# Kernel optimization log

Measured on AMD Instinct MI355X. Metric: run time of the kernel, lower is better.

## Reference

```python
import jax, jax.numpy as jnp
import numpy as np

D = 200; K = 10; NHEAD = 5; HDIM = 40; ANS = 2; THRESH = 0.4; GHEAD = 5; GC = 2
B = 8; L = 80; R = 64

def _lin(x, W, b):
    return x @ W + b

def _ln(x, g, b):
    m = jnp.mean(x, -1, keepdims=True)
    v = jnp.var(x, -1, keepdims=True)
    return (x - m) / jnp.sqrt(v + 1e-5) * g + b

def _sparsemax(z):
    # sparsemax along last axis (Martins & Astudillo)
    zs = -jnp.sort(-z, axis=-1)
    k = jnp.arange(1, z.shape[-1] + 1, dtype=z.dtype)
    cs = jnp.cumsum(zs, -1)
    supp = jnp.sum((1.0 + k * zs) > cs, -1, keepdims=True)
    tau = (jnp.take_along_axis(cs, supp - 1, -1) - 1.0) / supp.astype(z.dtype)
    return jnp.maximum(z - tau, 0.0)

def _pair(a, b):
    # a [B,n,d], b [B,m,d] -> [B,n*m,4d] feature cat [a, b, a*b, a-b]
    Bn, n, d = a.shape; m = b.shape[1]
    a1 = jnp.broadcast_to(a[:, :, None, :], (Bn, n, m, d))
    b1 = jnp.broadcast_to(b[:, None, :, :], (Bn, n, m, d))
    return jnp.concatenate([a1, b1, a1 * b1, a1 - b1], -1).reshape(Bn, n * m, 4 * d)

def _topk_sel(E, s, mask):
    # select top-K instances by score (masked)
    s = jnp.where(mask, s, -jnp.inf)
    _, idx = jax.lax.top_k(s, K)
    return jnp.take_along_axis(E, idx[:, :, None], axis=1)

def _mco(x, W_attn, b_attn, W_ff1, b_ff1, W_ff2, b_ff2, ln_g, ln_b):
    # transformer encoder layer: MHA + FFN, post-norm (dropout off at eval)
    Bn, N, d = x.shape
    q = _lin(x, W_attn[0], b_attn[0]).reshape(Bn, N, NHEAD, HDIM)
    k = _lin(x, W_attn[1], b_attn[1]).reshape(Bn, N, NHEAD, HDIM)
    v = _lin(x, W_attn[2], b_attn[2]).reshape(Bn, N, NHEAD, HDIM)
    att = jax.nn.softmax(jnp.einsum('bnhk,bmhk->bhnm', q, k) / np.float32(np.sqrt(HDIM)), axis=-1)
    o = jnp.einsum('bhnm,bmhk->bnhk', att, v).reshape(Bn, N, d)
    x = _ln(x + _lin(o, W_attn[3], b_attn[3]), ln_g[0], ln_b[0])
    f = _lin(jax.nn.relu(_lin(x, W_ff1, b_ff1)), W_ff2, b_ff2)
    return _ln(x + f, ln_g[1], ln_b[1])

def _forward(imgs, encoded_texts, mask_T, mask_TT, mask_TV, adj,
             answer_set, Wt, bt, Wi1, bi1, Wi2, bi2, Wgc, bgc, Wps, bps, Wts, bts,
             W_single, b_single, W_pair1, b_pair1, W_pair2, b_pair2, W_topk, b_topk,
             clues, W_clue1, b_clue1, W_ans1, b_ans1, W_inst2, b_inst2, W_ans2, b_ans2,
             W_attn, b_attn, W_ff1, b_ff1, W_ff2, b_ff2, ln_g, ln_b,
             W_guide, b_guide, W_at1, b_at1, W_at2, b_at2):
    imgs_0 = jax.nn.relu(_lin(jax.nn.relu(_lin(imgs, Wi1, bi1)), Wi2, bi2))  # ImageEncoder 768->500->200
    texts_0 = _lin(encoded_texts, Wt, bt)                                    # TextEncoder 768->200
    Bn, l, _ = texts_0.shape
    r = imgs_0.shape[1]
    ones_V = jnp.ones((Bn, r), bool)
    ones_VV = jnp.ones((Bn, r * r), bool)
    out = []
    for gc_i in range(GC):
        def pair_mlp(f, i):
            return jax.nn.relu(_lin(jax.nn.relu(_lin(f, W_pair1[i], b_pair1[i])), W_pair2[i], b_pair2[i]))
        def score(E, i):
            return jax.nn.relu(E @ W_topk[i] + b_topk[i])
        # five modality streams
        E_T = jax.nn.relu(_lin(texts_0, W_single[0], b_single[0]))
        E_V = jax.nn.relu(_lin(imgs_0, W_single[1], b_single[1]))
        E_TT = pair_mlp(_pair(texts_0, texts_0), 0)
        E_TV = pair_mlp(_pair(texts_0, imgs_0), 1)
        E_VV = pair_mlp(_pair(imgs_0, imgs_0), 2)
        E_T_k = _topk_sel(E_T, score(E_T, 0), mask_T)
        E_V_k = _topk_sel(E_V, score(E_V, 1), ones_V)
        E_TT_k = _topk_sel(E_TT, score(E_TT, 2), mask_TT)
        E_TV_k = _topk_sel(E_TV, score(E_TV, 3), mask_TV)
        E_VV_k = _topk_sel(E_VV, score(E_VV, 4), ones_VV)
        # clue binding: attend selected instances onto per-stream clue banks, condition on answer set
        ans1 = _lin(answer_set, W_ans1, b_ans1)
        def bind(Ek, c):
            att = jax.nn.softmax(jnp.einsum('bkd,cd->bkc', Ek, c), -1)
            bound = jnp.einsum('bkc,cd->bkd', att, c)
            return jax.nn.relu(_lin(bound, W_clue1, b_clue1)[:, :, None, :] + ans1[None, None])
        preds = jnp.concatenate([bind(E_T_k, clues[0]), bind(E_V_k, clues[1]), bind(E_TT_k, clues[2]), bind(E_TV_k, clues[3]), bind(E_VV_k, clues[4])], axis=1)  # [B,5K,A,D]
        E_cat = jnp.concatenate([E_T_k, E_V_k, E_TT_k, E_TV_k, E_VV_k], 1)
        E4 = jnp.broadcast_to(E_cat[:, :, None, :], preds.shape)
        inst_score = jnp.einsum('bnad,ad->bna', _lin(E4, W_inst2, b_inst2), _lin(answer_set, W_ans2, b_ans2))
        preds_ = jnp.stack([_mco(preds[:, :, a, :], W_attn, b_attn, W_ff1, b_ff1, W_ff2, b_ff2, ln_g, ln_b) for a in range(ANS)], axis=2)
        feat = jnp.concatenate([E4, preds, E4 - preds, E4 * preds], -1)
        atoms = jax.nn.sigmoid(_lin(jax.nn.relu(_lin(feat, W_at1, b_at1)), W_at2, b_at2))[..., 0]
        atoms = jnp.transpose(atoms, (2, 0, 1))  # [A,B,5K]
        # global text/image embeddings for guide scores
        I_score = jax.nn.softmax(imgs_0 @ Wps + bps, -1)
        T_score = jax.nn.softmax(texts_0 @ Wts + bts, -1)
        I_emb = jnp.einsum('brd,br->bd', imgs_0, I_score)
        T_emb = jnp.einsum('bld,bl->bd', texts_0, T_score)
        E_IT = pair_mlp(jnp.concatenate([T_emb, I_emb, T_emb * I_emb, T_emb - I_emb], -1), 1)
        heads = []
        for gi in range(GHEAD):
            g1 = jnp.einsum('bnad,d->bna', preds_, W_guide[2 * gi]) + b_guide[2 * gi]
            g2 = (E_IT @ W_guide[2 * gi + 1] + b_guide[2 * gi + 1])[:, None, None]
            fcs = _sparsemax(g1 * g2) * _sparsemax(inst_score)
            fcs = _sparsemax(jnp.transpose(fcs, (2, 0, 1)))  # [A,B,5K], sparsemax over instances
            flag = fcs >= THRESH
            mprod = jnp.prod(jnp.where(flag, atoms, 1.0), -1)  # conjunction over selected atoms
            vals, idx = jax.lax.top_k(fcs, 3)                  # fallback: top-3 atoms weighted by score
            fb = jnp.prod(jnp.take_along_axis(atoms, idx, -1) * vals, -1)
            heads.append(jnp.where(jnp.any(flag, -1), mprod, fb))  # [A,B]
        out.append(jnp.max(jnp.stack(heads, -1), -1))  # max over guide heads -> [A,B]
        # graph convolution refines text+image node features for next iteration
        graph = jnp.concatenate([texts_0, imgs_0], 1)
        graph = jax.nn.relu(jnp.einsum('bnm,bmd->bnd', adj, graph) @ Wgc[gc_i] + bgc[gc_i])
        texts_0 = graph[:, :l, :]
        imgs_0 = graph[:, l:, :]
    return jnp.stack(out)  # [GC, A, B]

def setup_inputs():
    ks = jax.random.split(jax.random.key(0), 64)
    def rn(i, shape, s=0.05):
        return jax.random.normal(ks[i], shape, dtype=jnp.float32) * s
    inp = {}
    inp['imgs'] = rn(0, (B, R, 768), 1.0)
    inp['encoded_texts'] = rn(1, (B, L, 768), 1.0)
    inp['mask_batch_T'] = jnp.ones((B, L), dtype=bool)
    inp['mask_batch_TT'] = jnp.ones((B, L * L), dtype=bool)
    inp['mask_batch_TV'] = jnp.ones((B, L * R), dtype=bool)
    inp['adj_matrix'] = jax.random.uniform(ks[2], (B, L + R, L + R), dtype=jnp.float32) / (L + R)
    inp['word_len'] = jax.random.randint(ks[3], (B,), 1, L)
    inp['word_spans'] = jax.random.randint(ks[4], (B, L, 2), 0, L)
    inp['answer_set'] = rn(5, (ANS, D), 0.5)
    inp['Wt'] = rn(6, (768, D)); inp['bt'] = rn(7, (D,))
    inp['Wi1'] = rn(8, (768, 500)); inp['bi1'] = rn(9, (500,))
    inp['Wi2'] = rn(10, (500, D)); inp['bi2'] = rn(11, (D,))
    inp['Wgc'] = rn(12, (GC, D, D)); inp['bgc'] = rn(13, (GC, D))
    inp['Wps'] = rn(14, (D,), 0.5); inp['bps'] = rn(15, ())
    inp['Wts'] = rn(16, (D,), 0.5); inp['bts'] = rn(17, ())
    inp['W_single'] = rn(18, (2, D, D)); inp['b_single'] = rn(19, (2, D))
    inp['W_pair1'] = rn(20, (3, 4 * D, 2 * D)); inp['b_pair1'] = rn(21, (3, 2 * D))
    inp['W_pair2'] = rn(22, (3, 2 * D, D)); inp['b_pair2'] = rn(23, (3, D))
    inp['W_topk'] = rn(24, (5, D), 0.5); inp['b_topk'] = rn(25, (5,))
    inp['clues'] = rn(26, (5, 5, D), 0.5)
    inp['W_clue1'] = rn(27, (D, D)); inp['b_clue1'] = rn(28, (D,))
    inp['W_ans1'] = rn(29, (D, D)); inp['b_ans1'] = rn(30, (D,))
    inp['W_inst2'] = rn(31, (D, D)); inp['b_inst2'] = rn(32, (D,))
    inp['W_ans2'] = rn(33, (D, D)); inp['b_ans2'] = rn(34, (D,))
    inp['W_attn'] = rn(35, (4, D, D)); inp['b_attn'] = rn(36, (4, D))
    inp['W_ff1'] = rn(37, (D, 2 * D)); inp['b_ff1'] = rn(38, (2 * D,))
    inp['W_ff2'] = rn(39, (2 * D, D)); inp['b_ff2'] = rn(40, (D,))
    inp['ln_g'] = jnp.ones((2, D), jnp.float32); inp['ln_b'] = jnp.zeros((2, D), jnp.float32)
    inp['W_guide'] = rn(41, (2 * GHEAD, D), 0.5); inp['b_guide'] = rn(42, (2 * GHEAD,))
    inp['W_at1'] = rn(43, (4 * D, 2 * D)); inp['b_at1'] = rn(44, (2 * D,))
    inp['W_at2'] = rn(45, (2 * D, 1)); inp['b_at2'] = rn(46, (1,))
    return inp

def reference(imgs, encoded_texts, mask_batch_T, mask_batch_TT, mask_batch_TV, adj_matrix, word_len, word_spans,
              answer_set, Wt, bt, Wi1, bi1, Wi2, bi2, Wgc, bgc, Wps, bps, Wts, bts,
              W_single, b_single, W_pair1, b_pair1, W_pair2, b_pair2, W_topk, b_topk,
              clues, W_clue1, b_clue1, W_ans1, b_ans1, W_inst2, b_inst2, W_ans2, b_ans2,
              W_attn, b_attn, W_ff1, b_ff1, W_ff2, b_ff2, ln_g, ln_b,
              W_guide, b_guide, W_at1, b_at1, W_at2, b_at2):
    # word_len / word_spans are consumed by the (simplified) TextEncoder pooling; not needed here
    return _forward(imgs, encoded_texts, mask_batch_T, mask_batch_TT, mask_batch_TV, adj_matrix,
                    answer_set, Wt, bt, Wi1, bi1, Wi2, bi2, Wgc, bgc, Wps, bps, Wts, bts,
                    W_single, b_single, W_pair1, b_pair1, W_pair2, b_pair2, W_topk, b_topk,
                    clues, W_clue1, b_clue1, W_ans1, b_ans1, W_inst2, b_inst2, W_ans2, b_ans2,
                    W_attn, b_attn, W_ff1, b_ff1, W_ff2, b_ff2, ln_g, ln_b,
                    W_guide, b_guide, W_at1, b_at1, W_at2, b_at2)
```

## Files before the change

kernel.cpp:

```cpp
#include <hip/hip_runtime.h>
#include <hip/hip_bf16.h>


__device__ __forceinline__ void sparsemax2(float z0, float z1, float& o0, float& o1) {
  float S0 = (z1 > z0) ? z1 : 0.f;
  float S1 = (z0 > z1) ? z0 : 0.f;
  float cz0 = (z1 > z0) ? z0 : 0.f;
  float cz1 = (z0 > z1) ? z1 : 0.f;
  bool c0 = (1.f + cz0) > S0;
  bool c1 = (1.f + cz1) > S1;
  float supp = (c0 ? 1.f : 0.f) + (c1 ? 1.f : 0.f);
  float Ss   = (c0 ? z0  : 0.f) + (c1 ? z1  : 0.f);
  float tau = (Ss - 1.f) / supp;
  o0 = fmaxf(z0 - tau, 0.f);
  o1 = fmaxf(z1 - tau, 0.f);
}

__global__ __launch_bounds__(256) void gemm_k(
    const float* __restrict__ A, const float* __restrict__ Bw,
    const float* __restrict__ bias, float* __restrict__ C,
    int M, int N, int K, long sA, long sB, long sC, int act)
{
  int batch = blockIdx.z;
  A  += (long)batch * sA;
  Bw += (long)batch * sB;
  C  += (long)batch * sC;
  __shared__ float As[32][33];
  __shared__ float Bs[32][33];
  int tid = threadIdx.x;
  int tx = tid & 15, ty = tid >> 4;
  int row0 = blockIdx.y * 32, col0 = blockIdx.x * 32;
  float acc00 = 0.f, acc01 = 0.f, acc10 = 0.f, acc11 = 0.f;
  for (int k0 = 0; k0 < K; k0 += 32) {
    for (int i = tid; i < 1024; i += 256) {
      int r = i >> 5, c = i & 31;
      int ar = row0 + r, ac = k0 + c;
      As[r][c] = (ar < M && ac < K) ? A[(long)ar * K + ac] : 0.f;
      int br = k0 + r, bc = col0 + c;
      Bs[r][c] = (br < K && bc < N) ? Bw[(long)br * N + bc] : 0.f;
    }
    __syncthreads();
#pragma unroll
    for (int kk = 0; kk < 32; ++kk) {
      float a0 = As[ty * 2][kk], a1 = As[ty * 2 + 1][kk];
      float b0 = Bs[kk][tx * 2], b1 = Bs[kk][tx * 2 + 1];
      acc00 += a0 * b0; acc01 += a0 * b1; acc10 += a1 * b0; acc11 += a1 * b1;
    }
    __syncthreads();
  }
  int r0 = row0 + ty * 2, c0 = col0 + tx * 2;
#define STORE_(rr, cc, v)                                        \
  if ((rr) < M && (cc) < N) {                                    \
    float t_ = (v) + (bias ? bias[cc] : 0.f);                    \
    if (act) t_ = fmaxf(t_, 0.f);                                \
    C[(long)(rr) * N + (cc)] = t_;                               \
  }
  STORE_(r0, c0, acc00); STORE_(r0, c0 + 1, acc01);
  STORE_(r0 + 1, c0, acc10); STORE_(r0 + 1, c0 + 1, acc11);
#undef STORE_
}

__global__ void wab_kernel(const float* __restrict__ P1, float* __restrict__ Wa,
                           float* __restrict__ Wb) {
  int idx = blockIdx.x * 256 + threadIdx.x;
  if (idx >= 240000) return;
  int t = idx / 80000, r2 = idx % 80000;
  int d = r2 / 400, k = r2 % 400;
  long base = (long)t * 320000;
  float wd = P1[base + (long)(600 + d) * 400 + k];
  Wa[idx] = P1[base + (long)d * 400 + k] + wd;
  Wb[idx] = P1[base + (long)(200 + d) * 400 + k] - wd;
}

__global__ void ans_kernel(const float* __restrict__ as, const float* __restrict__ W1,
                           const float* __restrict__ b1, const float* __restrict__ W2,
                           const float* __restrict__ b2, float* __restrict__ ans1,
                           float* __restrict__ ans2) {
  int idx = blockIdx.x * 256 + threadIdx.x;
  if (idx >= 400) return;
  int a = idx / 200, d = idx % 200;
  float a1 = b1[d], a2 = b2[d];
  for (int k = 0; k < 200; ++k) {
    float av = as[a * 200 + k];
    a1 += av * W1[k * 200 + d];
    a2 += av * W2[k * 200 + d];
  }
  ans1[idx] = a1;
  ans2[idx] = a2;
}

__global__ void rowdot_kernel(const float* __restrict__ E, const float* __restrict__ Wt,
                              const float* __restrict__ bt, int g, float* __restrict__ s,
                              int rows) {
  int r = blockIdx.x * 256 + threadIdx.x;
  if (r >= rows) return;
  const float* e = E + (long)r * 200;
  const float* w = Wt + g * 200;
  float acc = bt[g];
  for (int d = 0; d < 200; ++d) acc += e[d] * w[d];
  s[r] = fmaxf(acc, 0.f);
}

__global__ __launch_bounds__(256) void pair_score_kernel(
    const float* __restrict__ Arows, int an, const float* __restrict__ Brows, int bm,
    const float* __restrict__ At, const float* __restrict__ Bt,
    const float* __restrict__ Wc, const float* __restrict__ W2,
    const float* __restrict__ b2, const float* __restrict__ wt,
    const float* __restrict__ btk, int gidx, float* __restrict__ scores)
{
  const int tid = threadIdx.x;
  const int b = blockIdx.y;
  const int nTJ = bm >> 3;
  const int i0 = (blockIdx.x / nTJ) * 8;
  const int j0 = (blockIdx.x % nTJ) * 8;

  Arows += (long)b * an * 200;
  Brows += (long)b * bm * 200;
  At += (long)b * an * 400;
  Bt += (long)b * bm * 400;
  scores += (long)b * an * bm;

  __shared__ __align__(16) float pdbuf[13056];
  __shared__ __align__(16) float stg[3200];

  const int tp = tid >> 4;
  const int tk = tid & 15;
  const int tc = tid & 15;

  for (int idx = tid; idx < 12800; idx += 256) {
    int p = idx / 200, d = idx - p * 200;
    pdbuf[p * 204 + d] = Arows[(long)(i0 + (p >> 3)) * 200 + d] *
                         Brows[(long)(j0 + (p & 7)) * 200 + d];
  }

  float acc[4][25];
#pragma unroll
  for (int q = 0; q < 4; ++q)
#pragma unroll
    for (int kk = 0; kk < 25; ++kk) acc[q][kk] = 0.f;

  float wreg[7];
#pragma unroll
  for (int l = 0; l < 7; ++l) {
    int idx = tid + l * 256;
    if (idx < 1600) wreg[l] = Wc[(long)(idx / 400) * 400 + idx % 400];
  }
#pragma unroll
  for (int l = 0; l < 7; ++l) {
    int idx = tid + l * 256;
    if (idx < 1600) stg[idx] = wreg[l];
  }
  __syncthreads();

  for (int ph = 0; ph < 50; ++ph) {
    const int cur = ph & 1, nxt = cur ^ 1;
    if (ph < 49) {
#pragma unroll
      for (int l = 0; l < 7; ++l) {
        int idx = tid + l * 256;
        if (idx < 1600)
          wreg[l] = Wc[(long)((ph + 1) * 4 + idx / 400) * 400 + idx % 400];
      }
    }
    float pdq[4][4];
#pragma unroll
    for (int q = 0; q < 4; ++q) {
      const float4 v = *reinterpret_cast<const float4*>(
          &pdbuf[(tp * 4 + q) * 204 + ph * 4]);
      pdq[q][0] = v.x; pdq[q][1] = v.y; pdq[q][2] = v.z; pdq[q][3] = v.w;
    }
#pragma unroll
    for (int dd = 0; dd < 4; ++dd) {
      const float* wrow = &stg[cur * 1600 + dd * 400 + tk * 25];
#pragma unroll
      for (int kk = 0; kk < 25; ++kk) {
        const float wv = wrow[kk];
        acc[0][kk] = fmaf(pdq[0][dd], wv, acc[0][kk]);
        acc[1][kk] = fmaf(pdq[1][dd], wv, acc[1][kk]);
        acc[2][kk] = fmaf(pdq[2][dd], wv, acc[2][kk]);
        acc[3][kk] = fmaf(pdq[3][dd], wv, acc[3][kk]);
      }
    }
    if (ph < 49) {
#pragma unroll
      for (int l = 0; l < 7; ++l) {
        int idx = tid + l * 256;
        if (idx < 1600) stg[nxt * 1600 + idx] = wreg[l];
      }
    }
    __syncthreads();
  }

  {
    const float* Ar = &At[(long)(i0 + (tp >> 1)) * 400 + tk * 25];
#pragma unroll
    for (int q = 0; q < 4; ++q) {
      const float* Br = &Bt[(long)(j0 + ((tp & 1) * 4 + q)) * 400 + tk * 25];
#pragma unroll
      for (int kk = 0; kk < 25; ++kk)
        acc[q][kk] = fmaxf(acc[q][kk] + Ar[kk] + Br[kk], 0.f);
    }
  }

  float acc2[4][13];
#pragma unroll
  for (int q = 0; q < 4; ++q)
#pragma unroll
    for (int cc = 0; cc < 13; ++cc) acc2[q][cc] = 0.f;

  float4* const H4 = reinterpret_cast<float4*>(pdbuf);

  for (int P = 0; P < 2; ++P) {
    if ((tk >> 3) == P) {
      const int klbase = (tk & 7) * 25;
#pragma unroll
      for (int kk = 0; kk < 25; ++kk) {
        const int kl = klbase + kk;
        float4 hv = make_float4(acc[0][kk], acc[1][kk], acc[2][kk], acc[3][kk]);
        H4[kl * 16 + (tp ^ ((kl & 7) * 2))] = hv;
      }
    }
#pragma unroll
    for (int l = 0; l < 7; ++l) {
      int idx = tid + l * 256;
      if (idx < 1600) {
        int g = idx >= 800, j = idx - g * 800;
        wreg[l] = W2[(long)(P * 200 + g * 4 + (j & 3)) * 200 + (j >> 2)];
      }
    }
#pragma unroll
    for (int l = 0; l < 7; ++l) {
      int idx = tid + l * 256;
      if (idx < 1600) stg[idx] = wreg[l];
    }
    __syncthreads();

    for (int ch = 0; ch < 25; ++ch) {
      const int cur = ch & 1, nxt = cur ^ 1;
      if (ch < 24) {
#pragma unroll
        for (int l = 0; l < 7; ++l) {
          int idx = tid + l * 256;
          if (idx < 1600) {
            int g = idx >= 800, j = idx - g * 800;
            wreg[l] = W2[(long)(P * 200 + (ch + 1) * 8 + g * 4 + (j & 3)) * 200 +
                         (j >> 2)];
          }
        }
      }
#pragma unroll
      for (int g = 0; g < 2; ++g) {
        const int r0 = ch * 8 + g * 4;
        float4 h0 = H4[(r0 + 0) * 16 + (tp ^ (((g * 4 + 0) & 7) * 2))];
        float4 h1 = H4[(r0 + 1) * 16 + (tp ^ (((g * 4 + 1) & 7) * 2))];
        float4 h2 = H4[(r0 + 2) * 16 + (tp ^ (((g * 4 + 2) & 7) * 2))];
        float4 h3 = H4[(r0 + 3) * 16 + (tp ^ (((g * 4 + 3) & 7) * 2))];
        const float4* S4 = reinterpret_cast<const float4*>(&stg[cur * 1600 + g * 800]);
#pragma unroll
        for (int cc = 0; cc < 13; ++cc) {
          if (!(cc == 12 && tc >= 8)) {
            const float4 wv = S4[tc + 16 * cc];
            acc2[0][cc] += h0.x * wv.x + h1.x * wv.y + h2.x * wv.z + h3.x * wv.w;
            acc2[1][cc] += h0.y * wv.x + h1.y * wv.y + h2.y * wv.z + h3.y * wv.w;
            acc2[2][cc] += h0.z * wv.x + h1.z * wv.y + h2.z * wv.z + h3.z * wv.w;
            acc2[3][cc] += h0.w * wv.x + h1.w * wv.y + h2.w * wv.z + h3.w * wv.w;
          }
        }
      }
      if (ch < 24) {
#pragma unroll
        for (int l = 0; l < 7; ++l) {
          int idx = tid + l * 256;
          if (idx < 1600) stg[nxt * 1600 + idx] = wreg[l];
        }
      }
      __syncthreads();
    }
  }

  float part[4] = {0.f, 0.f, 0.f, 0.f};
#pragma unroll
  for (int cc = 0; cc < 13; ++cc) {
    if (!(cc == 12 && tc >= 8)) {
      const int c = tc + 16 * cc;
      const float bb = b2[c], ww = wt[c];
#pragma unroll
      for (int q = 0; q < 4; ++q)
        part[q] += fmaxf(acc2[q][cc] + bb, 0.f) * ww;
    }
  }
#pragma unroll
  for (int off = 1; off < 16; off <<= 1) {
#pragma unroll
    for (int q = 0; q < 4; ++q) part[q] += __shfl_xor(part[q], off, 64);
  }
  if ((tid & 15) == 0) {
    const float bt_ = btk[gidx];
#pragma unroll
    for (int q = 0; q < 4; ++q) {
      const int p = tp * 4 + q;
      scores[(long)(i0 + (p >> 3)) * bm + (j0 + (p & 7))] = fmaxf(part[q] + bt_, 0.f);
    }
  }
}

__global__ void topk_kernel(const float* __restrict__ sT, const float* __restrict__ sV,
                            const float* __restrict__ sTT, const float* __restrict__ sTV,
                            const float* __restrict__ sVV, int* __restrict__ topIdx) {
  int g = blockIdx.x, b = blockIdx.y, tid = threadIdx.x;
  const float* src; int len;
  switch (g) {
    case 0: src = sT + b * 80; len = 80; break;
    case 1: src = sV + b * 64; len = 64; break;
    case 2: src = sTT + b * 6400; len = 6400; break;
    case 3: src = sTV + b * 5120; len = 5120; break;
    default: src = sVV + b * 4096; len = 4096; break;
  }
  __shared__ float sbuf[6400];
  __shared__ float rv[256];
  __shared__ int ri[256];
  for (int i = tid; i < len; i += 256) sbuf[i] = src[i];
  __syncthreads();
  for (int r = 0; r < 10; ++r) {
    float bv = -1e30f; int bi = 0x7fffffff;
    for (int i = tid; i < len; i += 256) {
      float v = sbuf[i];
      if (v > bv) { bv = v; bi = i; }
    }
    rv[tid] = bv; ri[tid] = bi;
    __syncthreads();
    for (int s = 128; s > 0; s >>= 1) {
      if (tid < s) {
        if (rv[tid + s] > rv[tid] || (rv[tid + s] == rv[tid] && ri[tid + s] < ri[tid])) {
          rv[tid] = rv[tid + s]; ri[tid] = ri[tid + s];
        }
      }
      __syncthreads();
    }
    if (tid == 0) {
      topIdx[(g * 8 + b) * 10 + r] = ri[0];
      sbuf[ri[0]] = -1e30f;
    }
    __syncthreads();
  }
}

__global__ void gather_kernel(
    const int* __restrict__ topIdx, const float* __restrict__ ETf,
    const float* __restrict__ EVf, const float* __restrict__ texts0,
    const float* __restrict__ imgs0, const float* __restrict__ AtTT,
    const float* __restrict__ BtTT, const float* __restrict__ AtTV,
    const float* __restrict__ BtTV, const float* __restrict__ AtVV,
    const float* __restrict__ BtVV, const float* __restrict__ W_pair1,
    const float* __restrict__ W_pair2, const float* __restrict__ b_pair2,
    float* __restrict__ E_cat)
{
  int n = blockIdx.x, b = blockIdx.y, tid = threadIdx.x;
  int g = n / 10, r = n % 10;
  int idx = topIdx[(g * 8 + b) * 10 + r];
  float* out = E_cat + ((long)(b * 50 + n)) * 200;
  if (g == 0) {
    for (int d = tid; d < 200; d += 256) out[d] = ETf[((long)(b * 80 + idx)) * 200 + d];
    return;
  }
  if (g == 1) {
    for (int d = tid; d < 200; d += 256) out[d] = EVf[((long)(b * 64 + idx)) * 200 + d];
    return;
  }
  int t = g - 2;
  int m = (t == 0) ? 80 : 64;
  int i = idx / m, j = idx % m;
  const float* ar = (t == 2) ? imgs0 + ((long)(b * 64 + i)) * 200
                             : texts0 + ((long)(b * 80 + i)) * 200;
  const float* br = (t == 0) ? texts0 + ((long)(b * 80 + j)) * 200
                             : imgs0 + ((long)(b * 64 + j)) * 200;
  const float* Atp = ((t == 0) ? AtTT : (t == 1) ? AtTV : AtVV) +
                     ((long)(b * ((t == 2) ? 64 : 80) + i)) * 400;
  const float* Btp = ((t == 0) ? BtTT : (t == 1) ? BtTV : BtVV) +
                     ((long)(b * ((t == 0) ? 80 : 64) + j)) * 400;
  const float* Wc = W_pair1 + (long)t * 320000 + 160000;
  const float* W2 = W_pair2 + (long)t * 80000;
  const float* bb2 = b_pair2 + t * 200;
  __shared__ float pd[200];
  __shared__ float hh[400];
  for (int d = tid; d < 200; d += 256) pd[d] = ar[d] * br[d];
  __syncthreads();
  for (int k = tid; k < 400; k += 256) {
    float acc = Atp[k] + Btp[k];
    for (int d = 0; d < 200; ++d) acc += pd[d] * Wc[(long)d * 400 + k];
    hh[k] = fmaxf(acc, 0.f);
  }
  __syncthreads();
  for (int c = tid; c < 200; c += 256) {
    float acc = bb2[c];
    for (int k = 0; k < 400; ++k) acc += hh[k] * W2[(long)k * 200 + c];
    out[c] = fmaxf(acc, 0.f);
  }
}

__global__ void bind_kernel(const float* __restrict__ E_cat, const float* __restrict__ clues,
                            const float* __restrict__ W_clue1, const float* __restrict__ b_clue1,
                            const float* __restrict__ ans1, const float* __restrict__ W_inst2,
                            const float* __restrict__ b_inst2, const float* __restrict__ ans2,
                            float* __restrict__ preds, float* __restrict__ inst) {
  int n = blockIdx.x, b = blockIdx.y, tid = threadIdx.x;
  int g = n / 10;
  const float* e = E_cat + ((long)(b * 50 + n)) * 200;
  __shared__ float es[200], att[5], bound[200], vv[200], red[256];
  for (int d = tid; d < 200; d += 256) es[d] = e[d];
  __syncthreads();
  if (tid < 5) {
    const float* cl = clues + ((long)(g * 5 + tid)) * 200;
    float acc = 0.f;
    for (int d = 0; d < 200; ++d) acc += es[d] * cl[d];
    att[tid] = acc;
  }
  __syncthreads();
  if (tid == 0) {
    float mx = att[0];
    for (int c = 1; c < 5; ++c) mx = fmaxf(mx, att[c]);
    float s = 0.f;
    for (int c = 0; c < 5; ++c) { att[c] = expf(att[c] - mx); s += att[c]; }
    float inv = 1.f / s;
    for (int c = 0; c < 5; ++c) att[c] *= inv;
  }
  __syncthreads();
  if (tid < 200) {
    float acc = 0.f;
    for (int c = 0; c < 5; ++c) acc += att[c] * clues[((long)(g * 5 + c)) * 200 + tid];
    bound[tid] = acc;
  }
  __syncthreads();
  if (tid < 200) {
    float acc = b_clue1[tid];
    for (int k = 0; k < 200; ++k) acc += bound[k] * W_clue1[(long)k * 200 + tid];
    long rbase = ((long)(b * 50 + n)) * 2;
    preds[(rbase + 0) * 200 + tid] = fmaxf(acc + ans1[tid], 0.f);
    preds[(rbase + 1) * 200 + tid] = fmaxf(acc + ans1[200 + tid], 0.f);
    float a2 = b_inst2[tid];
    for (int k = 0; k < 200; ++k) a2 += es[k] * W_inst2[(long)k * 200 + tid];
    vv[tid] = a2;
  }
  __syncthreads();
  float p0 = 0.f, p1 = 0.f;
  for (int d = tid; d < 200; d += 256) {
    p0 += vv[d] * ans2[d];
    p1 += vv[d] * ans2[200 + d];
  }
  red[tid] = p0; __syncthreads();
  for (int s = 128; s > 0; s >>= 1) { if (tid < s) red[tid] += red[tid + s]; __syncthreads(); }
  if (tid == 0) inst[((long)(b * 50 + n)) * 2 + 0] = red[0];
  __syncthreads();
  red[tid] = p1; __syncthreads();
  for (int s = 128; s > 0; s >>= 1) { if (tid < s) red[tid] += red[tid + s]; __syncthreads(); }
  if (tid == 0) inst[((long)(b * 50 + n)) * 2 + 1] = red[0];
}

__global__ void attn_kernel(const float* __restrict__ Q, const float* __restrict__ K,
                            const float* __restrict__ V, float* __restrict__ O) {
  int h = blockIdx.x, a = blockIdx.y, b = blockIdx.z, tid = threadIdx.x;
  __shared__ float qs[50][40], ks[50][40], vs[50][40], ss[50][52];
  for (int idx = tid; idx < 2000; idx += 256) {
    int n = idx / 40, t = idx % 40;
    long base = ((long)((b * 50 + n) * 2 + a)) * 200 + h * 40 + t;
    qs[n][t] = Q[base]; ks[n][t] = K[base]; vs[n][t] = V[base];
  }
  __syncthreads();
  float sq = sqrtf(40.0f);
  for (int idx = tid; idx < 2500; idx += 256) {
    int n = idx / 50, m = idx % 50;
    float acc = 0.f;
    for (int t = 0; t < 40; ++t) acc += qs[n][t] * ks[m][t];
    ss[n][m] = acc / sq;
  }
  __syncthreads();
  if (tid < 50) {
    float mx = -1e30f;
    for (int m = 0; m < 50; ++m) mx = fmaxf(mx, ss[tid][m]);
    float s = 0.f;
    for (int m = 0; m < 50; ++m) { float e = expf(ss[tid][m] - mx); ss[tid][m] = e; s += e; }
    float inv = 1.f / s;
    for (int m = 0; m < 50; ++m) ss[tid][m] *= inv;
  }
  __syncthreads();
  for (int idx = tid; idx < 2000; idx += 256) {
    int n = idx / 40, t = idx % 40;
    float acc = 0.f;
    for (int m = 0; m < 50; ++m) acc += ss[n][m] * vs[m][t];
    O[((long)((b * 50 + n) * 2 + a)) * 200 + h * 40 + t] = acc;
  }
}

__global__ void ln_kernel(const float* __restrict__ X, const float* __restrict__ Rres,
                          const float* __restrict__ g, const float* __restrict__ bb,
                          float* __restrict__ out) {
  int row = blockIdx.x, tid = threadIdx.x;
  __shared__ float red[256];
  __shared__ float mv[2];
  float v = 0.f;
  if (tid < 200) v = X[(long)row * 200 + tid] + Rres[(long)row * 200 + tid];
  red[tid] = (tid < 200) ? v : 0.f;
  __syncthreads();
  for (int s = 128; s > 0; s >>= 1) { if (tid < s) red[tid] += red[tid + s]; __syncthreads(); }
  if (tid == 0) mv[0] = red[0] / 200.f;
  __syncthreads();
  float m = mv[0];
  float dv = (tid < 200) ? (v - m) : 0.f;
  red[tid] = dv * dv;
  __syncthreads();
  for (int s = 128; s > 0; s >>= 1) { if (tid < s) red[tid] += red[tid + s]; __syncthreads(); }
  if (tid == 0) mv[1] = red[0] / 200.f;
  __syncthreads();
  if (tid < 200) {
    float scale = 1.f / sqrtf(mv[1] + 1e-5f);
    out[(long)row * 200 + tid] = (v - m) * scale * g[tid] + bb[tid];
  }
}

__global__ void feat_kernel(const float* __restrict__ E_cat, const float* __restrict__ preds,
                            float* __restrict__ feat) {
  int row = blockIdx.x, tid = threadIdx.x;
  int bn = row >> 1;
  const float* e = E_cat + (long)bn * 200;
  const float* p = preds + (long)row * 200;
  float* f = feat + (long)row * 800;
  for (int d = tid; d < 200; d += 256) {
    float ev = e[d], pv = p[d];
    f[d] = ev; f[200 + d] = pv; f[400 + d] = ev - pv; f[600 + d] = ev * pv;
  }
}

__global__ void atoms_kernel(const float* __restrict__ bufAt, const float* __restrict__ W_at2,
                             const float* __restrict__ b_at2, float* __restrict__ atoms) {
  int row = blockIdx.x, tid = threadIdx.x;
  __shared__ float red[256];
  float p = 0.f;
  for (int k = tid; k < 400; k += 256) p += bufAt[(long)row * 400 + k] * W_at2[k];
  red[tid] = p;
  __syncthreads();
  for (int s = 128; s > 0; s >>= 1) { if (tid < s) red[tid] += red[tid + s]; __syncthreads(); }
  if (tid == 0) atoms[row] = 1.f / (1.f + expf(-(red[0] + b_at2[0])));
}

__global__ void emb_kernel(const float* __restrict__ texts0, const float* __restrict__ imgs0,
                           const float* __restrict__ Wts, const float* __restrict__ bts,
                           const float* __restrict__ Wps, const float* __restrict__ bps,
                           const float* __restrict__ W_pair1, const float* __restrict__ b_pair1,
                           const float* __restrict__ W_pair2, const float* __restrict__ b_pair2,
                           float* __restrict__ E_IT) {
  int b = blockIdx.x, tid = threadIdx.x;
  __shared__ float tsc[80], isc[64], f[800], hh[400];
  if (tid < 80) {
    float acc = bts[0];
    for (int d = 0; d < 200; ++d) acc += texts0[((long)(b * 80 + tid)) * 200 + d] * Wts[d];
    tsc[tid] = acc;
  }
  if (tid >= 128 && tid < 192) {
    int r = tid - 128;
    float acc = bps[0];
    for (int d = 0; d < 200; ++d) acc += imgs0[((long)(b * 64 + r)) * 200 + d] * Wps[d];
    isc[r] = acc;
  }
  __syncthreads();
  if (tid == 0) {
    float mx = -1e30f;
    for (int i = 0; i < 80; ++i) mx = fmaxf(mx, tsc[i]);
    float s = 0.f;
    for (int i = 0; i < 80; ++i) { tsc[i] = expf(tsc[i] - mx); s += tsc[i]; }
    float inv = 1.f / s;
    for (int i = 0; i < 80; ++i) tsc[i] *= inv;
  }
  if (tid == 1) {
    float mx = -1e30f;
    for (int i = 0; i < 64; ++i) mx = fmaxf(mx, isc[i]);
    float s = 0.f;
    for (int i = 0; i < 64; ++i) { isc[i] = expf(isc[i] - mx); s += isc[i]; }
    float inv = 1.f / s;
    for (int i = 0; i < 64; ++i) isc[i] *= inv;
  }
  __syncthreads();
  if (tid < 200) {
    float te = 0.f, ie = 0.f;
    for (int i = 0; i < 80; ++i) te += tsc[i] * texts0[((long)(b * 80 + i)) * 200 + tid];
    for (int r = 0; r < 64; ++r) ie += isc[r] * imgs0[((long)(b * 64 + r)) * 200 + tid];
    f[tid] = te; f[200 + tid] = ie; f[400 + tid] = te * ie; f[600 + tid] = te - ie;
  }
  __syncthreads();
  const float* W1 = W_pair1 + 320000;
  for (int k = tid; k < 400; k += 256) {
    float acc = b_pair1[400 + k];
    for (int d = 0; d < 800; ++d) acc += f[d] * W1[(long)d * 400 + k];
    hh[k] = fmaxf(acc, 0.f);
  }
  __syncthreads();
  const float* W2 = W_pair2 + 80000;
  for (int c = tid; c < 200; c += 256) {
    float acc = b_pair2[200 + c];
    for (int k = 0; k < 400; ++k) acc += hh[k] * W2[(long)k * 200 + c];
    E_IT[b * 200 + c] = fmaxf(acc, 0.f);
  }
}

__global__ void head_kernel(const float* __restrict__ predsM, const float* __restrict__ inst,
                            const float* __restrict__ atoms, const float* __restrict__ E_IT,
                            const float* __restrict__ W_guide, const float* __restrict__ b_guide,
                            float* __restrict__ dout, int gc) {
  int b = blockIdx.x, tid = threadIdx.x;
  __shared__ float smI[50][2], fcs1[50][2], fcs[2][50], atm[50][2], condv[2][50];
  __shared__ float g2v, tau[2], hm[2];
  if (tid < 50) {
    long base = ((long)(b * 50 + tid)) * 2;
    float i0 = inst[base + 0], i1 = inst[base + 1];
    sparsemax2(i0, i1, smI[tid][0], smI[tid][1]);
    atm[tid][0] = atoms[base + 0];
    atm[tid][1] = atoms[base + 1];
  }
  if (tid == 0) { hm[0] = -1e30f; hm[1] = -1e30f; }
  __syncthreads();
  for (int gi = 0; gi < 5; ++gi) {
    if (tid == 0) {
      float acc = b_guide[2 * gi + 1];
      const float* wg = W_guide + (2 * gi + 1) * 200;
      for (int d = 0; d < 200; ++d) acc += E_IT[b * 200 + d] * wg[d];
      g2v = acc;
    }
    __syncthreads();
    if (tid < 50) {
      const float* wg = W_guide + 2 * gi * 200;
      float z0 = b_guide[2 * gi], z1 = b_guide[2 * gi];
      const float* p0 = predsM + (((long)(b * 50 + tid)) * 2 + 0) * 200;
      const float* p1 = p0 + 200;
      for (int d = 0; d < 200; ++d) { z0 += p0[d] * wg[d]; z1 += p1[d] * wg[d]; }
      z0 *= g2v; z1 *= g2v;
      float s0, s1;
      sparsemax2(z0, z1, s0, s1);
      fcs1[tid][0] = s0 * smI[tid][0];
      fcs1[tid][1] = s1 * smI[tid][1];
    }
    __syncthreads();
    if (tid < 100) {
      int a = tid / 50, n = tid % 50;
      float z = fcs1[n][a];
      int c = 0; float S = 0.f;
      for (int m = 0; m < 50; ++m) {
        float zm = fcs1[m][a];
        if (zm > z) { c++; S += zm; }
      }
      condv[a][n] = ((1.f + (float)c * z) > S) ? 1.f : 0.f;
    }
    __syncthreads();
    if (tid < 2) {
      float supp = 0.f, Ss = 0.f;
      for (int n = 0; n < 50; ++n)
        if (condv[tid][n] > 0.f) { supp += 1.f; Ss += fcs1[n][tid]; }
      tau[tid] = (Ss - 1.f) / supp;
    }
    __syncthreads();
    if (tid < 100) {
      int a = tid / 50, n = tid % 50;
      fcs[a][n] = fmaxf(fcs1[n][a] - tau[a], 0.f);
    }
    __syncthreads();
    if (tid < 2) {
      int a = tid;
      bool anyF = false;
      float mp = 1.f;
      for (int n = 0; n < 50; ++n) {
        if (fcs[a][n] >= 0.4f) { anyF = true; mp *= atm[n][a]; }
      }
      int p0 = -1, p1 = -1;
      float fb = 1.f;
      for (int t3 = 0; t3 < 3; ++t3) {
        float bv = -1e30f; int bi = -1;
        for (int n = 0; n < 50; ++n) {
          if (n == p0 || n == p1) continue;
          float v = fcs[a][n];
          if (v > bv) { bv = v; bi = n; }
        }
        if (t3 == 0) p0 = bi; else if (t3 == 1) p1 = bi;
        fb *= atm[bi][a] * bv;
      }
      float head = anyF ? mp : fb;
      hm[a] = fmaxf(hm[a], head);
    }
    __syncthreads();
  }
  if (tid < 2) dout[gc * 16 + tid * 8 + b] = hm[tid];
}

__global__ void graph_pack(const float* __restrict__ texts0, const float* __restrict__ imgs0,
                           float* __restrict__ gin) {
  int row = blockIdx.x, tid = threadIdx.x;
  int b = row / 144, rr = row % 144;
  const float* src = (rr < 80) ? texts0 + ((long)(b * 80 + rr)) * 200
                               : imgs0 + ((long)(b * 64 + rr - 80)) * 200;
  float* dst = gin + (long)row * 200;
  if (tid < 200) dst[tid] = src[tid];
}

__global__ void graph_unpack(const float* __restrict__ gout, float* __restrict__ texts0,
                             float* __restrict__ imgs0) {
  int row = blockIdx.x, tid = threadIdx.x;
  int b = row / 144, rr = row % 144;
  const float* src = gout + (long)row * 200;
  float* dst = (rr < 80) ? texts0 + ((long)(b * 80 + rr)) * 200
                         : imgs0 + ((long)(b * 64 + rr - 80)) * 200;
  if (tid < 200) dst[tid] = src[tid];
}

extern "C" void kernel_launch(void* const* d_in, const int* in_sizes, int n_in,
                              void* d_out, int out_size, void* d_ws, size_t ws_size,
                              hipStream_t stream) {
  (void)in_sizes; (void)n_in; (void)out_size; (void)ws_size;
  const float* imgs = (const float*)d_in[0];
  const float* etexts = (const float*)d_in[1];
  const float* adj = (const float*)d_in[5];
  const float* answer_set = (const float*)d_in[8];
  const float* Wt = (const float*)d_in[9];
  const float* bt = (const float*)d_in[10];
  const float* Wi1 = (const float*)d_in[11];
  const float* bi1 = (const float*)d_in[12];
  const float* Wi2 = (const float*)d_in[13];
  const float* bi2 = (const float*)d_in[14];
  const float* Wgc = (const float*)d_in[15];
  const float* bgc = (const float*)d_in[16];
  const float* Wps = (const float*)d_in[17];
  const float* bps = (const float*)d_in[18];
  const float* Wts = (const float*)d_in[19];
  const float* bts = (const float*)d_in[20];
  const float* W_single = (const float*)d_in[21];
  const float* b_single = (const float*)d_in[22];
  const float* W_pair1 = (const float*)d_in[23];
  const float* b_pair1 = (const float*)d_in[24];
  const float* W_pair2 = (const float*)d_in[25];
  const float* b_pair2 = (const float*)d_in[26];
  const float* W_topk = (const float*)d_in[27];
  const float* b_topk = (const float*)d_in[28];
  const float* clues = (const float*)d_in[29];
  const float* W_clue1 = (const float*)d_in[30];
  const float* b_clue1 = (const float*)d_in[31];
  const float* W_ans1 = (const float*)d_in[32];
  const float* b_ans1 = (const float*)d_in[33];
  const float* W_inst2 = (const float*)d_in[34];
  const float* b_inst2 = (const float*)d_in[35];
  const float* W_ans2 = (const float*)d_in[36];
  const float* b_ans2 = (const float*)d_in[37];
  const float* W_attn = (const float*)d_in[38];
  const float* b_attn = (const float*)d_in[39];
  const float* W_ff1 = (const float*)d_in[40];
  const float* b_ff1 = (const float*)d_in[41];
  const float* W_ff2 = (const float*)d_in[42];
  const float* b_ff2 = (const float*)d_in[43];
  const float* ln_g = (const float*)d_in[44];
  const float* ln_b = (const float*)d_in[45];
  const float* W_guide = (const float*)d_in[46];
  const float* b_guide = (const float*)d_in[47];
  const float* W_at1 = (const float*)d_in[48];
  const float* b_at1 = (const float*)d_in[49];
  const float* W_at2 = (const float*)d_in[50];
  const float* b_at2 = (const float*)d_in[51];

  float* W = (float*)d_ws;
  size_t off = 0;
  auto A_ = [&](size_t n) { float* p = W + off; off += n; return p; };
  float* texts0 = A_(128000);
  float* imgs0 = A_(102400);
  float* tmp500 = A_(256000);
  float* Wa = A_(240000);
  float* Wb = A_(240000);
  float* AtTT = A_(256000);
  float* BtTT = A_(256000);
  float* AtTV = A_(256000);
  float* BtTV = A_(204800);
  float* AtVV = A_(204800);
  float* BtVV = A_(204800);
  float* ETf = A_(128000);
  float* EVf = A_(102400);
  float* sT = A_(640);
  float* sV = A_(512);
  float* sTT = A_(51200);
  float* sTV = A_(40960);
  float* sVV = A_(32768);
  float* E_cat = A_(80000);
  float* ans1 = A_(400);
  float* ans2 = A_(400);
  float* preds = A_(160000);
  float* inst = A_(800);
  float* bufQ = A_(160000);
  float* bufK = A_(160000);
  float* bufV = A_(160000);
  float* bufO = A_(160000);
  float* bufT1 = A_(160000);
  float* bufX1 = A_(160000);
  float* bufF1 = A_(320000);
  float* bufF2 = A_(160000);
  float* predsM = A_(160000);
  float* featb = A_(640000);
  float* bufAt = A_(320000);
  float* atoms = A_(800);
  float* E_IT = A_(1600);
  float* gin = A_(230400);
  float* tmpG = A_(230400);
  float* gout = A_(230400);
  int* topIdx = (int*)A_(400);

  dim3 blk(256);
  auto launch_gemm = [&](const float* Aa, const float* Bb, const float* bias, float* C,
                         int M, int N, int K, int act, int batch = 1, long sA = 0,
                         long sB = 0, long sC = 0) {
    dim3 g((N + 31) / 32, (M + 31) / 32, batch);
    gemm_k<<<g, blk, 0, stream>>>(Aa, Bb, bias, C, M, N, K, sA, sB, sC, act);
  };

  launch_gemm(imgs, Wi1, bi1, tmp500, 512, 500, 768, 1);
  launch_gemm(tmp500, Wi2, bi2, imgs0, 512, 200, 500, 1);
  launch_gemm(etexts, Wt, bt, texts0, 640, 200, 768, 0);
  wab_kernel<<<(240000 + 255) / 256, blk, 0, stream>>>(W_pair1, Wa, Wb);
  ans_kernel<<<2, blk, 0, stream>>>(answer_set, W_ans1, b_ans1, W_ans2, b_ans2, ans1, ans2);

  for (int gc = 0; gc < 2; ++gc) {
    launch_gemm(texts0, W_single, b_single, ETf, 640, 200, 200, 1);
    launch_gemm(imgs0, W_single + 40000, b_single + 200, EVf, 512, 200, 200, 1);
    rowdot_kernel<<<3, blk, 0, stream>>>(ETf, W_topk, b_topk, 0, sT, 640);
    rowdot_kernel<<<2, blk, 0, stream>>>(EVf, W_topk, b_topk, 1, sV, 512);
    launch_gemm(texts0, Wa, nullptr, AtTT, 640, 400, 200, 0);
    launch_gemm(texts0, Wb, b_pair1, BtTT, 640, 400, 200, 0);
    launch_gemm(texts0, Wa + 80000, nullptr, AtTV, 640, 400, 200, 0);
    launch_gemm(imgs0, Wb + 80000, b_pair1 + 400, BtTV, 512, 400, 200, 0);
    launch_gemm(imgs0, Wa + 160000, nullptr, AtVV, 512, 400, 200, 0);
    launch_gemm(imgs0, Wb + 160000, b_pair1 + 800, BtVV, 512, 400, 200, 0);
    pair_score_kernel<<<dim3(100, 8), blk, 0, stream>>>(
        texts0, 80, texts0, 80, AtTT, BtTT, W_pair1 + 160000, W_pair2, b_pair2,
        W_topk + 400, b_topk, 2, sTT);
    pair_score_kernel<<<dim3(80, 8), blk, 0, stream>>>(
        texts0, 80, imgs0, 64, AtTV, BtTV, W_pair1 + 480000, W_pair2 + 80000,
        b_pair2 + 200, W_topk + 600, b_topk, 3, sTV);
    pair_score_kernel<<<dim3(64, 8), blk, 0, stream>>>(
        imgs0, 64, imgs0, 64, AtVV, BtVV, W_pair1 + 800000, W_pair2 + 160000,
        b_pair2 + 400, W_topk + 800, b_topk, 4, sVV);
    topk_kernel<<<dim3(5, 8), blk, 0, stream>>>(sT, sV, sTT, sTV, sVV, topIdx);
    gather_kernel<<<dim3(50, 8), blk, 0, stream>>>(topIdx, ETf, EVf, texts0, imgs0, AtTT,
                                                   BtTT, AtTV, BtTV, AtVV, BtVV, W_pair1,
                                                   W_pair2, b_pair2, E_cat);
    bind_kernel<<<dim3(50, 8), blk, 0, stream>>>(E_cat, clues, W_clue1, b_clue1, ans1,
                                                 W_inst2, b_inst2, ans2, preds, inst);
    launch_gemm(preds, W_attn, b_attn, bufQ, 800, 200, 200, 0);
    launch_gemm(preds, W_attn + 40000, b_attn + 200, bufK, 800, 200, 200, 0);
    launch_gemm(preds, W_attn + 80000, b_attn + 400, bufV, 800, 200, 200, 0);
    attn_kernel<<<dim3(5, 2, 8), blk, 0, stream>>>(bufQ, bufK, bufV, bufO);
    launch_gemm(bufO, W_attn + 120000, b_attn + 600, bufT1, 800, 200, 200, 0);
    ln_kernel<<<800, blk, 0, stream>>>(preds, bufT1, ln_g, ln_b, bufX1);
    launch_gemm(bufX1, W_ff1, b_ff1, bufF1, 800, 400, 200, 1);
    launch_gemm(bufF1, W_ff2, b_ff2, bufF2, 800, 200, 400, 0);
    ln_kernel<<<800, blk, 0, stream>>>(bufX1, bufF2, ln_g + 200, ln_b + 200, predsM);
    feat_kernel<<<800, blk, 0, stream>>>(E_cat, preds, featb);
    launch_gemm(featb, W_at1, b_at1, bufAt, 800, 400, 800, 1);
    atoms_kernel<<<800, blk, 0, stream>>>(bufAt, W_at2, b_at2, atoms);
    emb_kernel<<<8, blk, 0, stream>>>(texts0, imgs0, Wts, bts, Wps, bps, W_pair1, b_pair1,
                                      W_pair2, b_pair2, E_IT);
    head_kernel<<<8, blk, 0, stream>>>(predsM, inst, atoms, E_IT, W_guide, b_guide,
                                       (float*)d_out, gc);
    if (gc == 0) {
      graph_pack<<<1152, blk, 0, stream>>>(texts0, imgs0, gin);
      launch_gemm(adj, gin, nullptr, tmpG, 144, 200, 144, 0, 8, 144 * 144, 144 * 200,
                  144 * 200);
      launch_gemm(tmpG, Wgc, bgc, gout, 1152, 200, 200, 1);
      graph_unpack<<<1152, blk, 0, stream>>>(gout, texts0, imgs0);
    }
  }
}
```

Before: 4.048 ms.

## Halve pair-score tile to 8x4 pairs for more blocks and occupancy

The pair-score kernel now handles 32 pairs per block instead of 64, doubling the grid and shrinking per-thread accumulators so that launch_bounds can request 4 blocks per SM. The Wc staging uses a padded 28-stride layout so weights can be read as float4, and the hidden buffer becomes an unswizzled float2 layout. The goal is better latency hiding and CU coverage. The cost is twice as many reads of the W_pair weights per pair, and possible register pressure or spilling under the tighter bound.

```diff
diff --git a/kernel.cpp b/kernel.cpp
--- a/kernel.cpp
+++ b/kernel.cpp
@@ -101,7 +101,7 @@
   s[r] = fmaxf(acc, 0.f);
 }
 
-__global__ __launch_bounds__(256) void pair_score_kernel(
+__global__ __launch_bounds__(256, 4) void pair_score_kernel(
     const float* __restrict__ Arows, int an, const float* __restrict__ Brows, int bm,
     const float* __restrict__ At, const float* __restrict__ Bt,
     const float* __restrict__ Wc, const float* __restrict__ W2,
@@ -110,9 +110,9 @@
 {
   const int tid = threadIdx.x;
   const int b = blockIdx.y;
-  const int nTJ = bm >> 3;
+  const int nTJ = bm >> 2;
   const int i0 = (blockIdx.x / nTJ) * 8;
-  const int j0 = (blockIdx.x % nTJ) * 8;
+  const int j0 = (blockIdx.x % nTJ) * 4;
 
   Arows += (long)b * an * 200;
   Brows += (long)b * bm * 200;
@@ -120,104 +120,110 @@
   Bt += (long)b * bm * 400;
   scores += (long)b * an * bm;
 
-  __shared__ __align__(16) float pdbuf[13056];
+  __shared__ __align__(16) float pdbuf[6800];
   __shared__ __align__(16) float stg[3200];
 
-  const int tp = tid >> 4;
+  const int tq = tid >> 4;
   const int tk = tid & 15;
-  const int tc = tid & 15;
-
-  for (int idx = tid; idx < 12800; idx += 256) {
+
+  for (int idx = tid; idx < 6400; idx += 256) {
     int p = idx / 200, d = idx - p * 200;
-    pdbuf[p * 204 + d] = Arows[(long)(i0 + (p >> 3)) * 200 + d] *
-                         Brows[(long)(j0 + (p & 7)) * 200 + d];
-  }
-
-  float acc[4][25];
-#pragma unroll
-  for (int q = 0; q < 4; ++q)
+    pdbuf[p * 200 + d] = Arows[(long)(i0 + (p >> 2)) * 200 + d] *
+                         Brows[(long)(j0 + (p & 3)) * 200 + d];
+  }
+
+  float acc[2][25];
+#pragma unroll
+  for (int q = 0; q < 2; ++q)
 #pragma unroll
     for (int kk = 0; kk < 25; ++kk) acc[q][kk] = 0.f;
 
-  float wreg[7];
-#pragma unroll
-  for (int l = 0; l < 7; ++l) {
+  float wreg[4];
+#pragma unroll
+  for (int l = 0; l < 4; ++l) {
     int idx = tid + l * 256;
-    if (idx < 1600) wreg[l] = Wc[(long)(idx / 400) * 400 + idx % 400];
-  }
-#pragma unroll
-  for (int l = 0; l < 7; ++l) {
+    if (idx < 896) {
+      int dd = idx / 448, rem = idx - dd * 448, tkx = rem / 28, kkx = rem - tkx * 28;
+      wreg[l] = (kkx < 25) ? Wc[(long)dd * 400 + tkx * 25 + kkx] : 0.f;
+    }
+  }
+#pragma unroll
+  for (int l = 0; l < 4; ++l) {
     int idx = tid + l * 256;
-    if (idx < 1600) stg[idx] = wreg[l];
-  }
-  __syncthreads();
-
-  for (int ph = 0; ph < 50; ++ph) {
+    if (idx < 896) stg[idx] = wreg[l];
+  }
+  __syncthreads();
+
+  for (int ph = 0; ph < 100; ++ph) {
     const int cur = ph & 1, nxt = cur ^ 1;
-    if (ph < 49) {
-#pragma unroll
-      for (int l = 0; l < 7; ++l) {
+    if (ph < 99) {
+#pragma unroll
+      for (int l = 0; l < 4; ++l) {
         int idx = tid + l * 256;
-        if (idx < 1600)
-          wreg[l] = Wc[(long)((ph + 1) * 4 + idx / 400) * 400 + idx % 400];
-      }
-    }
-    float pdq[4][4];
-#pragma unroll
-    for (int q = 0; q < 4; ++q) {
-      const float4 v = *reinterpret_cast<const float4*>(
-          &pdbuf[(tp * 4 + q) * 204 + ph * 4]);
-      pdq[q][0] = v.x; pdq[q][1] = v.y; pdq[q][2] = v.z; pdq[q][3] = v.w;
-    }
-#pragma unroll
-    for (int dd = 0; dd < 4; ++dd) {
-      const float* wrow = &stg[cur * 1600 + dd * 400 + tk * 25];
+        if (idx < 896) {
+          int dd = idx / 448, rem = idx - dd * 448, tkx = rem / 28, kkx = rem - tkx * 28;
+          wreg[l] = (kkx < 25)
+                        ? Wc[(long)((ph + 1) * 2 + dd) * 400 + tkx * 25 + kkx]
+                        : 0.f;
+        }
+      }
+    }
+    const float2 pq0 = *reinterpret_cast<const float2*>(&pdbuf[(tq * 2 + 0) * 200 + ph * 2]);
+    const float2 pq1 = *reinterpret_cast<const float2*>(&pdbuf[(tq * 2 + 1) * 200 + ph * 2]);
+#pragma unroll
+    for (int dd = 0; dd < 2; ++dd) {
+      const float* base = &stg[cur * 1600 + dd * 448 + tk * 28];
+      float w[25];
+      const float4* b4 = reinterpret_cast<const float4*>(base);
+#pragma unroll
+      for (int m = 0; m < 6; ++m) {
+        float4 v = b4[m];
+        w[m * 4 + 0] = v.x; w[m * 4 + 1] = v.y; w[m * 4 + 2] = v.z; w[m * 4 + 3] = v.w;
+      }
+      w[24] = base[24];
+      const float a0 = dd ? pq0.y : pq0.x;
+      const float a1 = dd ? pq1.y : pq1.x;
 #pragma unroll
       for (int kk = 0; kk < 25; ++kk) {
-        const float wv = wrow[kk];
-        acc[0][kk] = fmaf(pdq[0][dd], wv, acc[0][kk]);
-        acc[1][kk] = fmaf(pdq[1][dd], wv, acc[1][kk]);
-        acc[2][kk] = fmaf(pdq[2][dd], wv, acc[2][kk]);
-        acc[3][kk] = fmaf(pdq[3][dd], wv, acc[3][kk]);
-      }
-    }
-    if (ph < 49) {
-#pragma unroll
-      for (int l = 0; l < 7; ++l) {
+        acc[0][kk] = fmaf(a0, w[kk], acc[0][kk]);
+        acc[1][kk] = fmaf(a1, w[kk], acc[1][kk]);
+      }
+    }
+    if (ph < 99) {
+#pragma unroll
+      for (int l = 0; l < 4; ++l) {
         int idx = tid + l * 256;
-        if (idx < 1600) stg[nxt * 1600 + idx] = wreg[l];
+        if (idx < 896) stg[nxt * 1600 + idx] = wreg[l];
       }
     }
     __syncthreads();
   }
 
   {
-    const float* Ar = &At[(long)(i0 + (tp >> 1)) * 400 + tk * 25];
-#pragma unroll
-    for (int q = 0; q < 4; ++q) {
-      const float* Br = &Bt[(long)(j0 + ((tp & 1) * 4 + q)) * 400 + tk * 25];
+    const float* Ar = &At[(long)(i0 + (tq >> 1)) * 400 + tk * 25];
+#pragma unroll
+    for (int q = 0; q < 2; ++q) {
+      const float* Br = &Bt[(long)(j0 + 2 * (tq & 1) + q) * 400 + tk * 25];
 #pragma unroll
       for (int kk = 0; kk < 25; ++kk)
         acc[q][kk] = fmaxf(acc[q][kk] + Ar[kk] + Br[kk], 0.f);
     }
   }
 
-  float acc2[4][13];
-#pragma unroll
-  for (int q = 0; q < 4; ++q)
+  float acc2[2][13];
+#pragma unroll
+  for (int q = 0; q < 2; ++q)
 #pragma unroll
     for (int cc = 0; cc < 13; ++cc) acc2[q][cc] = 0.f;
 
-  float4* const H4 = reinterpret_cast<float4*>(pdbuf);
-
+  float wreg2[7];
   for (int P = 0; P < 2; ++P) {
     if ((tk >> 3) == P) {
       const int klbase = (tk & 7) * 25;
 #pragma unroll
       for (int kk = 0; kk < 25; ++kk) {
-        const int kl = klbase + kk;
-        float4 hv = make_float4(acc[0][kk], acc[1][kk], acc[2][kk], acc[3][kk]);
-        H4[kl * 16 + (tp ^ ((kl & 7) * 2))] = hv;
+        float2 hv = make_float2(acc[0][kk], acc[1][kk]);
+        *reinterpret_cast<float2*>(&pdbuf[(klbase + kk) * 34 + tq * 2]) = hv;
       }
     }
 #pragma unroll
@@ -225,13 +231,13 @@
       int idx = tid + l * 256;
       if (idx < 1600) {
         int g = idx >= 800, j = idx - g * 800;
-        wreg[l] = W2[(long)(P * 200 + g * 4 + (j & 3)) * 200 + (j >> 2)];
+        wreg2[l] = W2[(long)(P * 200 + g * 4 + (j & 3)) * 200 + (j >> 2)];
       }
     }
 #pragma unroll
     for (int l = 0; l < 7; ++l) {
       int idx = tid + l * 256;
-      if (idx < 1600) stg[idx] = wreg[l];
+      if (idx < 1600) stg[idx] = wreg2[l];
     }
     __syncthreads();
 
@@ -243,27 +249,25 @@
           int idx = tid + l * 256;
           if (idx < 1600) {
             int g = idx >= 800, j = idx - g * 800;
-            wreg[l] = W2[(long)(P * 200 + (ch + 1) * 8 + g * 4 + (j & 3)) * 200 +
-                         (j >> 2)];
+            wreg2[l] = W2[(long)(P * 200 + (ch + 1) * 8 + g * 4 + (j & 3)) * 200 +
+                          (j >> 2)];
           }
         }
       }
 #pragma unroll
       for (int g = 0; g < 2; ++g) {
         const int r0 = ch * 8 + g * 4;
-        float4 h0 = H4[(r0 + 0) * 16 + (tp ^ (((g * 4 + 0) & 7) * 2))];
-        float4 h1 = H4[(r0 + 1) * 16 + (tp ^ (((g * 4 + 1) & 7) * 2))];
-        float4 h2 = H4[(r0 + 2) * 16 + (tp ^ (((g * 4 + 2) & 7) * 2))];
-        float4 h3 = H4[(r0 + 3) * 16 + (tp ^ (((g * 4 + 3) & 7) * 2))];
+        const float2 h0 = *reinterpret_cast<const float2*>(&pdbuf[(r0 + 0) * 34 + tq * 2]);
+        const float2 h1 = *reinterpret_cast<const float2*>(&pdbuf[(r0 + 1) * 34 + tq * 2]);
+        const float2 h2 = *reinterpret_cast<const float2*>(&pdbuf[(r0 + 2) * 34 + tq * 2]);
+        const float2 h3 = *reinterpret_cast<const float2*>(&pdbuf[(r0 + 3) * 34 + tq * 2]);
         const float4* S4 = reinterpret_cast<const float4*>(&stg[cur * 1600 + g * 800]);
 #pragma unroll
         for (int cc = 0; cc < 13; ++cc) {
-          if (!(cc == 12 && tc >= 8)) {
-            const float4 wv = S4[tc + 16 * cc];
+          if (!(cc == 12 && tk >= 8)) {
+            const float4 wv = S4[tk + 16 * cc];
             acc2[0][cc] += h0.x * wv.x + h1.x * wv.y + h2.x * wv.z + h3.x * wv.w;
             acc2[1][cc] += h0.y * wv.x + h1.y * wv.y + h2.y * wv.z + h3.y * wv.w;
-            acc2[2][cc] += h0.z * wv.x + h1.z * wv.y + h2.z * wv.z + h3.z * wv.w;
-            acc2[3][cc] += h0.w * wv.x + h1.w * wv.y + h2.w * wv.z + h3.w * wv.w;
           }
         }
       }
@@ -271,35 +275,35 @@
 #pragma unroll
         for (int l = 0; l < 7; ++l) {
           int idx = tid + l * 256;
-          if (idx < 1600) stg[nxt * 1600 + idx] = wreg[l];
+          if (idx < 1600) stg[nxt * 1600 + idx] = wreg2[l];
         }
       }
       __syncthreads();
     }
   }
 
-  float part[4] = {0.f, 0.f, 0.f, 0.f};
+  float part[2] = {0.f, 0.f};
 #pragma unroll
   for (int cc = 0; cc < 13; ++cc) {
-    if (!(cc == 12 && tc >= 8)) {
-      const int c = tc + 16 * cc;
+    if (!(cc == 12 && tk >= 8)) {
+      const int c = tk + 16 * cc;
       const float bb = b2[c], ww = wt[c];
-#pragma unroll
-      for (int q = 0; q < 4; ++q)
-        part[q] += fmaxf(acc2[q][cc] + bb, 0.f) * ww;
+      part[0] += fmaxf(acc2[0][cc] + bb, 0.f) * ww;
+      part[1] += fmaxf(acc2[1][cc] + bb, 0.f) * ww;
     }
   }
 #pragma unroll
   for (int off = 1; off < 16; off <<= 1) {
-#pragma unroll
-    for (int q = 0; q < 4; ++q) part[q] += __shfl_xor(part[q], off, 64);
+    part[0] += __shfl_xor(part[0], off, 64);
+    part[1] += __shfl_xor(part[1], off, 64);
   }
   if ((tid & 15) == 0) {
     const float bt_ = btk[gidx];
-#pragma unroll
-    for (int q = 0; q < 4; ++q) {
-      const int p = tp * 4 + q;
-      scores[(long)(i0 + (p >> 3)) * bm + (j0 + (p & 7))] = fmaxf(part[q] + bt_, 0.f);
+    const int gi = i0 + (tq >> 1);
+#pragma unroll
+    for (int q = 0; q < 2; ++q) {
+      const int gj = j0 + 2 * (tq & 1) + q;
+      scores[(long)gi * bm + gj] = fmaxf(part[q] + bt_, 0.f);
     }
   }
 }
@@ -829,13 +833,13 @@
     launch_gemm(imgs0, Wb + 80000, b_pair1 + 400, BtTV, 512, 400, 200, 0);
     launch_gemm(imgs0, Wa + 160000, nullptr, AtVV, 512, 400, 200, 0);
     launch_gemm(imgs0, Wb + 160000, b_pair1 + 800, BtVV, 512, 400, 200, 0);
-    pair_score_kernel<<<dim3(100, 8), blk, 0, stream>>>(
+    pair_score_kernel<<<dim3(200, 8), blk, 0, stream>>>(
         texts0, 80, texts0, 80, AtTT, BtTT, W_pair1 + 160000, W_pair2, b_pair2,
         W_topk + 400, b_topk, 2, sTT);
-    pair_score_kernel<<<dim3(80, 8), blk, 0, stream>>>(
+    pair_score_kernel<<<dim3(160, 8), blk, 0, stream>>>(
         texts0, 80, imgs0, 64, AtTV, BtTV, W_pair1 + 480000, W_pair2 + 80000,
         b_pair2 + 200, W_topk + 600, b_topk, 3, sTV);
-    pair_score_kernel<<<dim3(64, 8), blk, 0, stream>>>(
+    pair_score_kernel<<<dim3(128, 8), blk, 0, stream>>>(
         imgs0, 64, imgs0, 64, AtVV, BtVV, W_pair1 + 800000, W_pair2 + 160000,
         b_pair2 + 400, W_topk + 800, b_topk, 4, sVV);
     topk_kernel<<<dim3(5, 8), blk, 0, stream>>>(sT, sV, sTT, sTV, sVV, topIdx);
```

Measured after the change: 6.726 ms. +66.2%, slower.
